# Performance work log

Hardware: AMD Instinct MI355X
Metric: run time of the kernel (lower is better)

## Reference

```python
import jax, jax.numpy as jnp
import numpy as np

B, T, N, F = 8, 64, 512, 32
G, C = 64, 64          # gcn_dim, tcn_dim
K, DIL = 2, 2          # TCN kernel_size, dilation
EPS = 1e-5


def setup_inputs() -> dict:
    key = jax.random.key(0)
    ks = jax.random.split(key, 20)
    s = 0.05
    return {
        "x": jax.random.normal(ks[0], (B, T, N, F), dtype=jnp.float32),
        "adj": jax.random.uniform(ks[1], (B, N, N), dtype=jnp.float32),
        # GraphConvLayer linear
        "gcn_w": jax.random.normal(ks[2], (F, G), dtype=jnp.float32) * s,
        "gcn_b": jnp.zeros((G,), dtype=jnp.float32),
        # TCN conv1 (weight-normed): v [out,in,K], g [out], bias [out]
        "v1": jax.random.normal(ks[3], (C, G, K), dtype=jnp.float32) * s,
        "g1": jnp.ones((C,), dtype=jnp.float32),
        "b1c": jnp.zeros((C,), dtype=jnp.float32),
        # TCN conv2
        "v2": jax.random.normal(ks[4], (C, C, K), dtype=jnp.float32) * s,
        "g2": jnp.ones((C,), dtype=jnp.float32),
        "b2c": jnp.zeros((C,), dtype=jnp.float32),
        # TemporalAttention: W1, W2 are [out,in] torch Linear layouts
        "W1": jax.random.normal(ks[5], (C, C), dtype=jnp.float32) * s,
        "b1": jnp.zeros((C,), dtype=jnp.float32),
        "W2": jax.random.normal(ks[6], (C, C), dtype=jnp.float32) * s,
        "b2": jnp.zeros((C,), dtype=jnp.float32),
        "Vw": jax.random.normal(ks[7], (C,), dtype=jnp.float32) * s,
        "Vb": jnp.zeros((), dtype=jnp.float32),
        # LayerNorm
        "ln_g": jnp.ones((C,), dtype=jnp.float32),
        "ln_b": jnp.zeros((C,), dtype=jnp.float32),
    }


def _wn(v, g):
    # torch weight_norm(dim=0): w = g * v / ||v|| over (in, K) per out-channel
    nrm = jnp.sqrt(jnp.sum(v * v, axis=(1, 2), keepdims=True))
    return g[:, None, None] * v / nrm


def _causal_conv(h, w, b, dilation):
    # h: [BN, Cin, T]; w: [Cout, Cin, K]; left-pad (K-1)*dilation == conv+chomp
    pad = (w.shape[2] - 1) * dilation
    y = jax.lax.conv_general_dilated(
        h, w, window_strides=(1,), padding=[(pad, 0)],
        rhs_dilation=(dilation,), dimension_numbers=("NCH", "OIH", "NCH"))
    return y + b[None, :, None]


def reference(x, adj, gcn_w, gcn_b, v1, g1, b1c, v2, g2, b2c,
              W1, b1, W2, b2, Vw, Vb, ln_g, ln_b):
    # ---- GCN (normalized adjacency is timestep-independent: compute once) ----
    adj_t = adj + jnp.eye(N, dtype=adj.dtype)[None]          # [B,N,N]
    deg = jnp.sum(adj_t, axis=2)                             # [B,N]
    d = jnp.where(deg > 0, jax.lax.rsqrt(jnp.where(deg > 0, deg, 1.0)), 0.0)
    norm_adj = d[:, :, None] * adj_t * d[:, None, :]         # [B,N,N]
    h = jnp.einsum("bij,btjf->btif", norm_adj, x)            # [B,T,N,F]
    gcn_out = jnp.einsum("btnf,fg->btng", h, gcn_w) + gcn_b  # [B,T,N,G]

    # ---- TCN over time, per (batch, node) channel sequence ----
    seq = gcn_out.transpose(0, 2, 3, 1).reshape(B * N, G, T)  # [BN,G,T]
    o1 = jax.nn.relu(_causal_conv(seq, _wn(v1, g1), b1c, DIL))
    o2 = jax.nn.relu(_causal_conv(o1, _wn(v2, g2), b2c, DIL))
    tcn = jax.nn.relu(o2 + seq)                               # shortcut=identity (G==C)
    tcn_out = tcn.reshape(B, N, C, T).transpose(0, 3, 1, 2)   # [B,T,N,C]

    # ---- Temporal attention per node (softmax over T) ----
    pre = jnp.tanh(jnp.einsum("btnc,dc->btnd", tcn_out, W1) + b1
                   + jnp.einsum("btnc,dc->btnd", tcn_out, W2) + b2)
    scores = jnp.einsum("btnd,d->btn", pre, Vw) + Vb          # [B,T,N]
    aw = jax.nn.softmax(scores, axis=1)                       # over T
    attn = jnp.einsum("btnc,btn->bnc", tcn_out, aw)           # [B,N,C]

    # ---- LayerNorm over channel dim ----
    mu = jnp.mean(attn, axis=-1, keepdims=True)
    var = jnp.mean((attn - mu) ** 2, axis=-1, keepdims=True)
    return (attn - mu) * jax.lax.rsqrt(var + EPS) * ln_g + ln_b
```

## Files before the change

kernel.cpp:

```cpp
#include <hip/hip_runtime.h>
#include <hip/hip_bf16.h>
#include <math.h>

#define B_ 8
#define T_ 64
#define N_ 512
#define F_ 32
#define G_ 64
#define C_ 64

typedef __attribute__((ext_vector_type(8))) short short8;
typedef __attribute__((ext_vector_type(4))) float f32x4;
typedef __attribute__((ext_vector_type(2))) float f32x2;

__device__ __forceinline__ unsigned short f2bf(float x) {
  unsigned u = __float_as_uint(x);
  u += 0x7fffu + ((u >> 16) & 1u);
  return (unsigned short)(u >> 16);
}
__device__ __forceinline__ float bf2f(unsigned short h) {
  return __uint_as_float(((unsigned)h) << 16);
}
__device__ __forceinline__ uint2 pack4(float a, float b, float c, float d) {
  uint2 r;
  r.x = (unsigned)f2bf(a) | ((unsigned)f2bf(b) << 16);
  r.y = (unsigned)f2bf(c) | ((unsigned)f2bf(d) << 16);
  return r;
}

__global__ __launch_bounds__(256) void deg_kernel(const float* __restrict__ adj,
                                                  float* __restrict__ d) {
  int row = blockIdx.x * 4 + (threadIdx.x >> 6);
  int lane = threadIdx.x & 63;
  const float* r = adj + (size_t)row * N_;
  float s = 0.f;
  #pragma unroll
  for (int j = lane; j < N_; j += 64) s += r[j];
  #pragma unroll
  for (int m = 1; m < 64; m <<= 1) s += __shfl_xor(s, m);
  if (lane == 0) {
    float deg = s + 1.0f;
    d[row] = (deg > 0.f) ? rsqrtf(deg) : 0.f;
  }
}

__global__ __launch_bounds__(256) void abf_kernel(const float* __restrict__ adj,
                                                  const float* __restrict__ d,
                                                  unsigned short* __restrict__ Abf) {
  int row = blockIdx.x * 4 + (threadIdx.x >> 6);
  int lane = threadIdx.x & 63;
  int b = row >> 9;
  int i = row & (N_ - 1);
  float di = d[row];
  const float* src = adj + (size_t)row * N_;
  unsigned short* dst = Abf + (size_t)row * N_;
  int j0 = lane * 8;
  float4 v0 = *(const float4*)(src + j0);
  float4 v1 = *(const float4*)(src + j0 + 4);
  float vals[8] = {v0.x, v0.y, v0.z, v0.w, v1.x, v1.y, v1.z, v1.w};
  unsigned short o[8];
  #pragma unroll
  for (int k = 0; k < 8; ++k) {
    int j = j0 + k;
    float a = vals[k] + ((i == j) ? 1.f : 0.f);
    o[k] = f2bf(a * di * d[b * N_ + j]);
  }
  uint4 pv;
  pv.x = (unsigned)o[0] | ((unsigned)o[1] << 16);
  pv.y = (unsigned)o[2] | ((unsigned)o[3] << 16);
  pv.z = (unsigned)o[4] | ((unsigned)o[5] << 16);
  pv.w = (unsigned)o[6] | ((unsigned)o[7] << 16);
  *(uint4*)(dst + j0) = pv;
}

__global__ __launch_bounds__(256) void xT_kernel(const float* __restrict__ x,
                                                 unsigned short* __restrict__ xT) {
  __shared__ float tile[64][33];
  int bt = blockIdx.x;
  int tid = threadIdx.x;
  const float* src = x + (size_t)bt * N_ * F_;
  unsigned short* dst = xT + (size_t)bt * F_ * N_;
  for (int j0 = 0; j0 < N_; j0 += 64) {
    #pragma unroll
    for (int kk = 0; kk < 2; ++kk) {
      int qq = tid + 256 * kk;
      int jl = qq >> 3, fc = qq & 7;
      float4 v = *(const float4*)(src + (size_t)(j0 + jl) * F_ + fc * 4);
      tile[jl][fc * 4 + 0] = v.x;
      tile[jl][fc * 4 + 1] = v.y;
      tile[jl][fc * 4 + 2] = v.z;
      tile[jl][fc * 4 + 3] = v.w;
    }
    __syncthreads();
    {
      int u = tid & 31, fr = tid >> 5;
      #pragma unroll
      for (int ff = 0; ff < 4; ++ff) {
        int f = fr + ff * 8;
        unsigned lo = f2bf(tile[2 * u][f]);
        unsigned hi = f2bf(tile[2 * u + 1][f]);
        ((unsigned*)(dst + (size_t)f * N_ + j0))[u] = lo | (hi << 16);
      }
    }
    __syncthreads();
  }
}

__global__ __launch_bounds__(256) void prep_kernel(
    const float* __restrict__ v1, const float* __restrict__ g1,
    const float* __restrict__ v2, const float* __restrict__ g2,
    const float* __restrict__ W1, const float* __restrict__ W2,
    const float* __restrict__ b1, const float* __restrict__ b2,
    const float* __restrict__ gcn_w,
    unsigned short* __restrict__ w1a, unsigned short* __restrict__ w1b,
    unsigned short* __restrict__ w2a, unsigned short* __restrict__ w2b,
    unsigned short* __restrict__ W12bf, float* __restrict__ b12,
    unsigned short* __restrict__ gw_bf) {
  int blk = blockIdx.x;
  int tid = threadIdx.x;
  if (blk < 128) {
    __shared__ float red[4];
    int c = blk & 63;
    const float* v = (blk < 64) ? v1 : v2;
    const float* g = (blk < 64) ? g1 : g2;
    unsigned short* wa = (blk < 64) ? w1a : w2a;
    unsigned short* wb = (blk < 64) ? w1b : w2b;
    float s = 0.f;
    if (tid < 128) { float t = v[c * 128 + tid]; s = t * t; }
    #pragma unroll
    for (int m = 1; m < 64; m <<= 1) s += __shfl_xor(s, m);
    if ((tid & 63) == 0) red[tid >> 6] = s;
    __syncthreads();
    float sc = g[c] / sqrtf(red[0] + red[1] + red[2] + red[3]);
    if (tid < 64) {
      int gg = tid;
      wa[c * 64 + gg] = f2bf(v[c * 128 + 2 * gg] * sc);
      wb[c * 64 + gg] = f2bf(v[c * 128 + 2 * gg + 1] * sc);
    }
  } else if (blk == 128) {
    for (int i = tid; i < 4096; i += 256) W12bf[i] = f2bf(W1[i] + W2[i]);
    if (tid < 64) b12[tid] = b1[tid] + b2[tid];
  } else {
    for (int i = tid; i < 2048; i += 256) {
      int g = i >> 5, f = i & 31;
      gw_bf[g * 32 + f] = f2bf(gcn_w[f * 64 + g]);
    }
  }
}

__global__ __launch_bounds__(256) void gcn_mfma_kernel(
    const unsigned short* __restrict__ Abf, const unsigned short* __restrict__ xT,
    unsigned short* __restrict__ h) {
  __shared__ unsigned short as_[64][40];
  __shared__ unsigned short xs_[64][40];

  int blk = blockIdx.x;
  int b = blk >> 8;
  int rem = blk & 255;
  int i0 = (rem >> 5) * 64;
  int t0 = (rem & 31) * 2;

  int tid = threadIdx.x;
  int l = tid & 63;
  int wq = tid >> 6;
  int wr = wq >> 1, wc = wq & 1;
  int lr = l & 15;
  int lk = (l >> 4) * 8;

  f32x4 acc00 = {0.f, 0.f, 0.f, 0.f}, acc01 = acc00, acc10 = acc00, acc11 = acc00;

  int srow = tid >> 2;
  int schunk = (tid & 3) * 8;

  const unsigned short* aSrc =
      Abf + ((size_t)(b * N_ + i0 + srow)) * N_ + schunk;
  int ttS = srow >> 5, fS = srow & 31;
  const unsigned short* xSrc =
      xT + ((size_t)((b * T_ + t0 + ttS) * F_ + fS)) * N_ + schunk;

  for (int j0 = 0; j0 < N_; j0 += 32) {
    *(short8*)&as_[srow][schunk] = *(const short8*)(aSrc + j0);
    *(short8*)&xs_[srow][schunk] = *(const short8*)(xSrc + j0);
    __syncthreads();
    short8 a0 = *(const short8*)&as_[wr * 32 + lr][lk];
    short8 a1 = *(const short8*)&as_[wr * 32 + 16 + lr][lk];
    short8 bb0 = *(const short8*)&xs_[wc * 32 + lr][lk];
    short8 bb1 = *(const short8*)&xs_[wc * 32 + 16 + lr][lk];
    acc00 = __builtin_amdgcn_mfma_f32_16x16x32_bf16(a0, bb0, acc00, 0, 0, 0);
    acc01 = __builtin_amdgcn_mfma_f32_16x16x32_bf16(a0, bb1, acc01, 0, 0, 0);
    acc10 = __builtin_amdgcn_mfma_f32_16x16x32_bf16(a1, bb0, acc10, 0, 0, 0);
    acc11 = __builtin_amdgcn_mfma_f32_16x16x32_bf16(a1, bb1, acc11, 0, 0, 0);
    __syncthreads();
  }

  int ibase = i0 + wr * 32 + (l >> 4) * 4;
  int cbase = wc * 32 + (l & 15);
  f32x4 accs[2][2] = {{acc00, acc01}, {acc10, acc11}};
  #pragma unroll
  for (int si = 0; si < 2; ++si)
    #pragma unroll
    for (int sc = 0; sc < 2; ++sc) {
      int col = cbase + sc * 16;
      int t = t0 + (col >> 5), f = col & 31;
      #pragma unroll
      for (int v = 0; v < 4; ++v) {
        int i = ibase + si * 16 + v;
        h[((size_t)((b * T_ + t) * N_ + i)) * F_ + f] = f2bf(accs[si][sc][v]);
      }
    }
}

__global__ __launch_bounds__(256) void tcn_attn_kernel(
    const unsigned short* __restrict__ h, const unsigned short* __restrict__ gw_bf,
    const float* __restrict__ gcn_b, const unsigned short* __restrict__ w1a,
    const unsigned short* __restrict__ w1b, const float* __restrict__ b1c,
    const unsigned short* __restrict__ w2a, const unsigned short* __restrict__ w2b,
    const float* __restrict__ b2c, const unsigned short* __restrict__ W12bf,
    const float* __restrict__ b12, const float* __restrict__ Vw,
    const float* __restrict__ Vb, const float* __restrict__ ln_g,
    const float* __restrict__ ln_b, float* __restrict__ out) {
  __shared__ unsigned short hS[64][40];
  __shared__ unsigned short seqS[66][72];
  __shared__ unsigned short o1S[66][72];
  __shared__ unsigned short tcnS[64][72];
  __shared__ float sp4[4][64];
  __shared__ float awS[64];

  int bn = blockIdx.x;
  int n = bn & (N_ - 1);
  int b = bn >> 9;
  int tid = threadIdx.x;
  int l = tid & 63;
  int q = tid >> 6;
  int lr = l & 15;
  int lk = (l >> 4) * 8;
  int c0 = q * 16 + (l >> 4) * 4;

  if (tid < 72) {
    seqS[0][tid] = 0; seqS[1][tid] = 0;
    o1S[0][tid] = 0;  o1S[1][tid] = 0;
  }
  {
    int t = tid >> 2, f0 = (tid & 3) * 8;
    *(short8*)&hS[t][f0] =
        *(const short8*)(h + ((size_t)((b * T_ + t) * N_ + n)) * F_ + f0);
  }
  __syncthreads();

  {
    short8 aG = *(const short8*)(gw_bf + (q * 16 + lr) * 32 + lk);
    float4 bias = *(const float4*)(gcn_b + c0);
    #pragma unroll
    for (int nt = 0; nt < 4; ++nt) {
      f32x4 acc = {0.f, 0.f, 0.f, 0.f};
      short8 bh = *(const short8*)&hS[nt * 16 + lr][lk];
      acc = __builtin_amdgcn_mfma_f32_16x16x32_bf16(aG, bh, acc, 0, 0, 0);
      uint2 pv = pack4(acc[0] + bias.x, acc[1] + bias.y,
                       acc[2] + bias.z, acc[3] + bias.w);
      *(uint2*)&seqS[nt * 16 + lr + 2][c0] = pv;
    }
  }
  __syncthreads();

  {
    short8 aA0 = *(const short8*)(w1a + (q * 16 + lr) * 64 + lk);
    short8 aA1 = *(const short8*)(w1a + (q * 16 + lr) * 64 + 32 + lk);
    short8 aB0 = *(const short8*)(w1b + (q * 16 + lr) * 64 + lk);
    short8 aB1 = *(const short8*)(w1b + (q * 16 + lr) * 64 + 32 + lk);
    float4 bias = *(const float4*)(b1c + c0);
    f32x4 acc[4];
    #pragma unroll
    for (int nt = 0; nt < 4; ++nt) acc[nt] = (f32x4){0.f, 0.f, 0.f, 0.f};
    #pragma unroll
    for (int nt = 0; nt < 4; ++nt) {
      int tr = nt * 16 + lr;
      short8 b00 = *(const short8*)&seqS[tr][lk];
      short8 b10 = *(const short8*)&seqS[tr + 2][lk];
      acc[nt] = __builtin_amdgcn_mfma_f32_16x16x32_bf16(aA0, b00, acc[nt], 0, 0, 0);
      acc[nt] = __builtin_amdgcn_mfma_f32_16x16x32_bf16(aB0, b10, acc[nt], 0, 0, 0);
    }
    #pragma unroll
    for (int nt = 0; nt < 4; ++nt) {
      int tr = nt * 16 + lr;
      short8 b01 = *(const short8*)&seqS[tr][32 + lk];
      short8 b11 = *(const short8*)&seqS[tr + 2][32 + lk];
      acc[nt] = __builtin_amdgcn_mfma_f32_16x16x32_bf16(aA1, b01, acc[nt], 0, 0, 0);
      acc[nt] = __builtin_amdgcn_mfma_f32_16x16x32_bf16(aB1, b11, acc[nt], 0, 0, 0);
    }
    #pragma unroll
    for (int nt = 0; nt < 4; ++nt) {
      uint2 pv = pack4(fmaxf(acc[nt][0] + bias.x, 0.f),
                       fmaxf(acc[nt][1] + bias.y, 0.f),
                       fmaxf(acc[nt][2] + bias.z, 0.f),
                       fmaxf(acc[nt][3] + bias.w, 0.f));
      *(uint2*)&o1S[nt * 16 + lr + 2][c0] = pv;
    }
  }
  __syncthreads();

  {
    short8 aA0 = *(const short8*)(w2a + (q * 16 + lr) * 64 + lk);
    short8 aA1 = *(const short8*)(w2a + (q * 16 + lr) * 64 + 32 + lk);
    short8 aB0 = *(const short8*)(w2b + (q * 16 + lr) * 64 + lk);
    short8 aB1 = *(const short8*)(w2b + (q * 16 + lr) * 64 + 32 + lk);
    float4 bias = *(const float4*)(b2c + c0);
    f32x4 acc[4];
    #pragma unroll
    for (int nt = 0; nt < 4; ++nt) acc[nt] = (f32x4){0.f, 0.f, 0.f, 0.f};
    #pragma unroll
    for (int nt = 0; nt < 4; ++nt) {
      int tr = nt * 16 + lr;
      short8 b00 = *(const short8*)&o1S[tr][lk];
      short8 b10 = *(const short8*)&o1S[tr + 2][lk];
      acc[nt] = __builtin_amdgcn_mfma_f32_16x16x32_bf16(aA0, b00, acc[nt], 0, 0, 0);
      acc[nt] = __builtin_amdgcn_mfma_f32_16x16x32_bf16(aB0, b10, acc[nt], 0, 0, 0);
    }
    #pragma unroll
    for (int nt = 0; nt < 4; ++nt) {
      int tr = nt * 16 + lr;
      short8 b01 = *(const short8*)&o1S[tr][32 + lk];
      short8 b11 = *(const short8*)&o1S[tr + 2][32 + lk];
      acc[nt] = __builtin_amdgcn_mfma_f32_16x16x32_bf16(aA1, b01, acc[nt], 0, 0, 0);
      acc[nt] = __builtin_amdgcn_mfma_f32_16x16x32_bf16(aB1, b11, acc[nt], 0, 0, 0);
    }
    #pragma unroll
    for (int nt = 0; nt < 4; ++nt) {
      int tr = nt * 16 + lr;
      uint2 sk = *(const uint2*)&seqS[tr + 2][c0];
      float s0 = bf2f((unsigned short)(sk.x & 0xffff));
      float s1 = bf2f((unsigned short)(sk.x >> 16));
      float s2 = bf2f((unsigned short)(sk.y & 0xffff));
      float s3 = bf2f((unsigned short)(sk.y >> 16));
      uint2 pv = pack4(fmaxf(fmaxf(acc[nt][0] + bias.x, 0.f) + s0, 0.f),
                       fmaxf(fmaxf(acc[nt][1] + bias.y, 0.f) + s1, 0.f),
                       fmaxf(fmaxf(acc[nt][2] + bias.z, 0.f) + s2, 0.f),
                       fmaxf(fmaxf(acc[nt][3] + bias.w, 0.f) + s3, 0.f));
      *(uint2*)&tcnS[tr][c0] = pv;
    }
  }
  __syncthreads();

  {
    short8 aW0 = *(const short8*)(W12bf + (q * 16 + lr) * 64 + lk);
    short8 aW1 = *(const short8*)(W12bf + (q * 16 + lr) * 64 + 32 + lk);
    float4 vwv = *(const float4*)(Vw + c0);
    float4 b12v = *(const float4*)(b12 + c0);
    #pragma unroll
    for (int nt = 0; nt < 4; ++nt) {
      int tr = nt * 16 + lr;
      f32x4 acc = {0.f, 0.f, 0.f, 0.f};
      short8 bb0 = *(const short8*)&tcnS[tr][lk];
      short8 bb1 = *(const short8*)&tcnS[tr][32 + lk];
      acc = __builtin_amdgcn_mfma_f32_16x16x32_bf16(aW0, bb0, acc, 0, 0, 0);
      acc = __builtin_amdgcn_mfma_f32_16x16x32_bf16(aW1, bb1, acc, 0, 0, 0);
      float p = 0.f;
      float bv[4] = {b12v.x, b12v.y, b12v.z, b12v.w};
      float vv[4] = {vwv.x, vwv.y, vwv.z, vwv.w};
      #pragma unroll
      for (int r = 0; r < 4; ++r) {
        float s = acc[r] + bv[r];
        float e = __expf(2.f * s);
        p += vv[r] * (1.f - 2.f / (e + 1.f));
      }
      p += __shfl_xor(p, 16);
      p += __shfl_xor(p, 32);
      if (l < 16) sp4[q][nt * 16 + l] = p;
    }
  }
  __syncthreads();

  if (tid < 64) {
    float s = sp4[0][l] + sp4[1][l] + sp4[2][l] + sp4[3][l] + Vb[0];
    float m = s;
    #pragma unroll
    for (int msk = 1; msk < 64; msk <<= 1) m = fmaxf(m, __shfl_xor(m, msk));
    float e = __expf(s - m);
    float su = e;
    #pragma unroll
    for (int msk = 1; msk < 64; msk <<= 1) su += __shfl_xor(su, msk);
    awS[l] = e / su;
  }
  __syncthreads();

  {
    float pa = 0.f;
    #pragma unroll
    for (int k = 0; k < 16; ++k)
      pa += bf2f(tcnS[q * 16 + k][l]) * awS[q * 16 + k];
    sp4[q][l] = pa;
  }
  __syncthreads();

  if (tid < 64) {
    int c = l;
    float a = sp4[0][c] + sp4[1][c] + sp4[2][c] + sp4[3][c];
    float su = a;
    #pragma unroll
    for (int msk = 1; msk < 64; msk <<= 1) su += __shfl_xor(su, msk);
    float mu = su * (1.f / 64.f);
    float dv = a - mu;
    float vv = dv * dv;
    #pragma unroll
    for (int msk = 1; msk < 64; msk <<= 1) vv += __shfl_xor(vv, msk);
    float rs = rsqrtf(vv * (1.f / 64.f) + 1e-5f);
    out[(size_t)bn * C_ + c] = dv * rs * ln_g[c] + ln_b[c];
  }
}

extern "C" void kernel_launch(void* const* d_in, const int* in_sizes, int n_in,
                              void* d_out, int out_size, void* d_ws, size_t ws_size,
                              hipStream_t stream) {
  (void)in_sizes; (void)n_in; (void)out_size; (void)ws_size;
  const float* x     = (const float*)d_in[0];
  const float* adj   = (const float*)d_in[1];
  const float* gcn_w = (const float*)d_in[2];
  const float* gcn_b = (const float*)d_in[3];
  const float* v1    = (const float*)d_in[4];
  const float* g1    = (const float*)d_in[5];
  const float* b1c   = (const float*)d_in[6];
  const float* v2    = (const float*)d_in[7];
  const float* g2    = (const float*)d_in[8];
  const float* b2c   = (const float*)d_in[9];
  const float* W1    = (const float*)d_in[10];
  const float* b1    = (const float*)d_in[11];
  const float* W2    = (const float*)d_in[12];
  const float* b2    = (const float*)d_in[13];
  const float* Vw    = (const float*)d_in[14];
  const float* Vb    = (const float*)d_in[15];
  const float* ln_g  = (const float*)d_in[16];
  const float* ln_b  = (const float*)d_in[17];
  float* out = (float*)d_out;

  char* ws = (char*)d_ws;
  unsigned short* h    = (unsigned short*)(ws);
  unsigned short* Abf  = (unsigned short*)(ws + 16777216);
  unsigned short* xT   = (unsigned short*)(ws + 20971520);
  float* dd            = (float*)(ws + 37748736);
  unsigned short* gw_bf= (unsigned short*)(ws + 37765120);
  unsigned short* w1a  = (unsigned short*)(ws + 37769216);
  unsigned short* w1b  = (unsigned short*)(ws + 37777408);
  unsigned short* w2a  = (unsigned short*)(ws + 37785600);
  unsigned short* w2b  = (unsigned short*)(ws + 37793792);
  unsigned short* W12bf= (unsigned short*)(ws + 37801984);
  float* b12           = (float*)(ws + 37810176);

  deg_kernel<<<(B_ * N_) / 4, 256, 0, stream>>>(adj, dd);
  abf_kernel<<<(B_ * N_) / 4, 256, 0, stream>>>(adj, dd, Abf);
  xT_kernel<<<B_ * T_, 256, 0, stream>>>(x, xT);
  prep_kernel<<<130, 256, 0, stream>>>(v1, g1, v2, g2, W1, W2, b1, b2, gcn_w,
                                       w1a, w1b, w2a, w2b, W12bf, b12, gw_bf);
  gcn_mfma_kernel<<<B_ * 256, 256, 0, stream>>>(Abf, xT, h);
  tcn_attn_kernel<<<B_ * N_, 256, 0, stream>>>(h, gw_bf, gcn_b, w1a, w1b, b1c,
                                               w2a, w2b, b2c, W12bf, b12, Vw,
                                               Vb, ln_g, ln_b, out);
}
```

Measured before the change: 187.3 us.

## Merge prep kernels, use direct global-to-LDS loads and packed bf16 converts

Folds the adjacency-normalisation, x-transpose and weight-prep kernels into one launch (1024+512+130 blocks), which removes two kernel launches and their serialization gaps. The GCN GEMM and TCN kernels now stage tiles with global_load_lds, skipping the register round trip, and LDS padding is dropped to fit that contiguous layout. Float-to-bf16 packing uses the hardware v_cvt_pk_bf16_f32 instruction. Unpadded LDS rows may add bank conflicts in the MFMA operand reads.

```diff
diff --git a/kernel.cpp b/kernel.cpp
--- a/kernel.cpp
+++ b/kernel.cpp
@@ -11,7 +11,6 @@
 
 typedef __attribute__((ext_vector_type(8))) short short8;
 typedef __attribute__((ext_vector_type(4))) float f32x4;
-typedef __attribute__((ext_vector_type(2))) float f32x2;
 
 __device__ __forceinline__ unsigned short f2bf(float x) {
   unsigned u = __float_as_uint(x);
@@ -21,12 +20,18 @@
 __device__ __forceinline__ float bf2f(unsigned short h) {
   return __uint_as_float(((unsigned)h) << 16);
 }
+__device__ __forceinline__ unsigned cvtpk(float lo, float hi) {
+  unsigned r;
+  asm("v_cvt_pk_bf16_f32 %0, %1, %2" : "=v"(r) : "v"(lo), "v"(hi));
+  return r;
+}
 __device__ __forceinline__ uint2 pack4(float a, float b, float c, float d) {
-  uint2 r;
-  r.x = (unsigned)f2bf(a) | ((unsigned)f2bf(b) << 16);
-  r.y = (unsigned)f2bf(c) | ((unsigned)f2bf(d) << 16);
-  return r;
-}
+  uint2 r; r.x = cvtpk(a, b); r.y = cvtpk(c, d); return r;
+}
+#define GLOAD16(gsrc, ldst)                                              \
+  __builtin_amdgcn_global_load_lds(                                      \
+      (const __attribute__((address_space(1))) unsigned int*)(gsrc),     \
+      (__attribute__((address_space(3))) unsigned int*)(ldst), 16, 0, 0)
 
 __global__ __launch_bounds__(256) void deg_kernel(const float* __restrict__ adj,
                                                   float* __restrict__ d) {
@@ -44,106 +49,104 @@
   }
 }
 
-__global__ __launch_bounds__(256) void abf_kernel(const float* __restrict__ adj,
-                                                  const float* __restrict__ d,
-                                                  unsigned short* __restrict__ Abf) {
-  int row = blockIdx.x * 4 + (threadIdx.x >> 6);
-  int lane = threadIdx.x & 63;
-  int b = row >> 9;
-  int i = row & (N_ - 1);
-  float di = d[row];
-  const float* src = adj + (size_t)row * N_;
-  unsigned short* dst = Abf + (size_t)row * N_;
-  int j0 = lane * 8;
-  float4 v0 = *(const float4*)(src + j0);
-  float4 v1 = *(const float4*)(src + j0 + 4);
-  float vals[8] = {v0.x, v0.y, v0.z, v0.w, v1.x, v1.y, v1.z, v1.w};
-  unsigned short o[8];
-  #pragma unroll
-  for (int k = 0; k < 8; ++k) {
-    int j = j0 + k;
-    float a = vals[k] + ((i == j) ? 1.f : 0.f);
-    o[k] = f2bf(a * di * d[b * N_ + j]);
-  }
-  uint4 pv;
-  pv.x = (unsigned)o[0] | ((unsigned)o[1] << 16);
-  pv.y = (unsigned)o[2] | ((unsigned)o[3] << 16);
-  pv.z = (unsigned)o[4] | ((unsigned)o[5] << 16);
-  pv.w = (unsigned)o[6] | ((unsigned)o[7] << 16);
-  *(uint4*)(dst + j0) = pv;
-}
-
-__global__ __launch_bounds__(256) void xT_kernel(const float* __restrict__ x,
-                                                 unsigned short* __restrict__ xT) {
-  __shared__ float tile[64][33];
-  int bt = blockIdx.x;
-  int tid = threadIdx.x;
-  const float* src = x + (size_t)bt * N_ * F_;
-  unsigned short* dst = xT + (size_t)bt * F_ * N_;
-  for (int j0 = 0; j0 < N_; j0 += 64) {
-    #pragma unroll
-    for (int kk = 0; kk < 2; ++kk) {
-      int qq = tid + 256 * kk;
-      int jl = qq >> 3, fc = qq & 7;
-      float4 v = *(const float4*)(src + (size_t)(j0 + jl) * F_ + fc * 4);
-      tile[jl][fc * 4 + 0] = v.x;
-      tile[jl][fc * 4 + 1] = v.y;
-      tile[jl][fc * 4 + 2] = v.z;
-      tile[jl][fc * 4 + 3] = v.w;
-    }
-    __syncthreads();
-    {
-      int u = tid & 31, fr = tid >> 5;
-      #pragma unroll
-      for (int ff = 0; ff < 4; ++ff) {
-        int f = fr + ff * 8;
-        unsigned lo = f2bf(tile[2 * u][f]);
-        unsigned hi = f2bf(tile[2 * u + 1][f]);
-        ((unsigned*)(dst + (size_t)f * N_ + j0))[u] = lo | (hi << 16);
-      }
-    }
-    __syncthreads();
-  }
-}
-
-__global__ __launch_bounds__(256) void prep_kernel(
+__global__ __launch_bounds__(256) void prep_all_kernel(
+    const float* __restrict__ adj, const float* __restrict__ d,
+    const float* __restrict__ x,
     const float* __restrict__ v1, const float* __restrict__ g1,
     const float* __restrict__ v2, const float* __restrict__ g2,
     const float* __restrict__ W1, const float* __restrict__ W2,
     const float* __restrict__ b1, const float* __restrict__ b2,
     const float* __restrict__ gcn_w,
+    unsigned short* __restrict__ Abf, unsigned short* __restrict__ xT,
     unsigned short* __restrict__ w1a, unsigned short* __restrict__ w1b,
     unsigned short* __restrict__ w2a, unsigned short* __restrict__ w2b,
     unsigned short* __restrict__ W12bf, float* __restrict__ b12,
     unsigned short* __restrict__ gw_bf) {
+  __shared__ float tile[64][33];
+  __shared__ float red[4];
   int blk = blockIdx.x;
   int tid = threadIdx.x;
-  if (blk < 128) {
-    __shared__ float red[4];
-    int c = blk & 63;
-    const float* v = (blk < 64) ? v1 : v2;
-    const float* g = (blk < 64) ? g1 : g2;
-    unsigned short* wa = (blk < 64) ? w1a : w2a;
-    unsigned short* wb = (blk < 64) ? w1b : w2b;
-    float s = 0.f;
-    if (tid < 128) { float t = v[c * 128 + tid]; s = t * t; }
-    #pragma unroll
-    for (int m = 1; m < 64; m <<= 1) s += __shfl_xor(s, m);
-    if ((tid & 63) == 0) red[tid >> 6] = s;
-    __syncthreads();
-    float sc = g[c] / sqrtf(red[0] + red[1] + red[2] + red[3]);
-    if (tid < 64) {
-      int gg = tid;
-      wa[c * 64 + gg] = f2bf(v[c * 128 + 2 * gg] * sc);
-      wb[c * 64 + gg] = f2bf(v[c * 128 + 2 * gg + 1] * sc);
-    }
-  } else if (blk == 128) {
-    for (int i = tid; i < 4096; i += 256) W12bf[i] = f2bf(W1[i] + W2[i]);
-    if (tid < 64) b12[tid] = b1[tid] + b2[tid];
+
+  if (blk < 1024) {
+    int row = blk * 4 + (tid >> 6);
+    int lane = tid & 63;
+    int b = row >> 9;
+    int i = row & (N_ - 1);
+    float di = d[row];
+    const float* src = adj + (size_t)row * N_;
+    unsigned short* dst = Abf + (size_t)row * N_;
+    int j0 = lane * 8;
+    float4 v0 = *(const float4*)(src + j0);
+    float4 v1v = *(const float4*)(src + j0 + 4);
+    float vals[8] = {v0.x, v0.y, v0.z, v0.w, v1v.x, v1v.y, v1v.z, v1v.w};
+    unsigned short o[8];
+    #pragma unroll
+    for (int k = 0; k < 8; ++k) {
+      int j = j0 + k;
+      float a = vals[k] + ((i == j) ? 1.f : 0.f);
+      o[k] = f2bf(a * di * d[b * N_ + j]);
+    }
+    uint4 pv;
+    pv.x = (unsigned)o[0] | ((unsigned)o[1] << 16);
+    pv.y = (unsigned)o[2] | ((unsigned)o[3] << 16);
+    pv.z = (unsigned)o[4] | ((unsigned)o[5] << 16);
+    pv.w = (unsigned)o[6] | ((unsigned)o[7] << 16);
+    *(uint4*)(dst + j0) = pv;
+  } else if (blk < 1536) {
+    int bt = blk - 1024;
+    const float* src = x + (size_t)bt * N_ * F_;
+    unsigned short* dst = xT + (size_t)bt * F_ * N_;
+    for (int j0 = 0; j0 < N_; j0 += 64) {
+      #pragma unroll
+      for (int kk = 0; kk < 2; ++kk) {
+        int qq = tid + 256 * kk;
+        int jl = qq >> 3, fc = qq & 7;
+        float4 v = *(const float4*)(src + (size_t)(j0 + jl) * F_ + fc * 4);
+        tile[jl][fc * 4 + 0] = v.x;
+        tile[jl][fc * 4 + 1] = v.y;
+        tile[jl][fc * 4 + 2] = v.z;
+        tile[jl][fc * 4 + 3] = v.w;
+      }
+      __syncthreads();
+      {
+        int u = tid & 31, fr = tid >> 5;
+        #pragma unroll
+        for (int ff = 0; ff < 4; ++ff) {
+          int f = fr + ff * 8;
+          ((unsigned*)(dst + (size_t)f * N_ + j0))[u] =
+              cvtpk(tile[2 * u][f], tile[2 * u + 1][f]);
+        }
+      }
+      __syncthreads();
+    }
   } else {
-    for (int i = tid; i < 2048; i += 256) {
-      int g = i >> 5, f = i & 31;
-      gw_bf[g * 32 + f] = f2bf(gcn_w[f * 64 + g]);
+    int pblk = blk - 1536;
+    if (pblk < 128) {
+      int c = pblk & 63;
+      const float* v = (pblk < 64) ? v1 : v2;
+      const float* g = (pblk < 64) ? g1 : g2;
+      unsigned short* wa = (pblk < 64) ? w1a : w2a;
+      unsigned short* wb = (pblk < 64) ? w1b : w2b;
+      float s = 0.f;
+      if (tid < 128) { float t = v[c * 128 + tid]; s = t * t; }
+      #pragma unroll
+      for (int m = 1; m < 64; m <<= 1) s += __shfl_xor(s, m);
+      if ((tid & 63) == 0) red[tid >> 6] = s;
+      __syncthreads();
+      float sc = g[c] / sqrtf(red[0] + red[1] + red[2] + red[3]);
+      if (tid < 64) {
+        int gg = tid;
+        wa[c * 64 + gg] = f2bf(v[c * 128 + 2 * gg] * sc);
+        wb[c * 64 + gg] = f2bf(v[c * 128 + 2 * gg + 1] * sc);
+      }
+    } else if (pblk == 128) {
+      for (int i = tid; i < 4096; i += 256) W12bf[i] = f2bf(W1[i] + W2[i]);
+      if (tid < 64) b12[tid] = b1[tid] + b2[tid];
+    } else {
+      for (int i = tid; i < 2048; i += 256) {
+        int g = i >> 5, f = i & 31;
+        gw_bf[g * 32 + f] = f2bf(gcn_w[f * 64 + g]);
+      }
     }
   }
 }
@@ -151,8 +154,8 @@
 __global__ __launch_bounds__(256) void gcn_mfma_kernel(
     const unsigned short* __restrict__ Abf, const unsigned short* __restrict__ xT,
     unsigned short* __restrict__ h) {
-  __shared__ unsigned short as_[64][40];
-  __shared__ unsigned short xs_[64][40];
+  __shared__ __align__(16) unsigned short as_[64][32];
+  __shared__ __align__(16) unsigned short xs_[64][32];
 
   int blk = blockIdx.x;
   int b = blk >> 8;
@@ -177,10 +180,12 @@
   int ttS = srow >> 5, fS = srow & 31;
   const unsigned short* xSrc =
       xT + ((size_t)((b * T_ + t0 + ttS) * F_ + fS)) * N_ + schunk;
+  unsigned short* aDst = &as_[0][0] + tid * 8;
+  unsigned short* xDst = &xs_[0][0] + tid * 8;
 
   for (int j0 = 0; j0 < N_; j0 += 32) {
-    *(short8*)&as_[srow][schunk] = *(const short8*)(aSrc + j0);
-    *(short8*)&xs_[srow][schunk] = *(const short8*)(xSrc + j0);
+    GLOAD16(aSrc + j0, aDst);
+    GLOAD16(xSrc + j0, xDst);
     __syncthreads();
     short8 a0 = *(const short8*)&as_[wr * 32 + lr][lk];
     short8 a1 = *(const short8*)&as_[wr * 32 + 16 + lr][lk];
@@ -219,10 +224,9 @@
     const float* __restrict__ b12, const float* __restrict__ Vw,
     const float* __restrict__ Vb, const float* __restrict__ ln_g,
     const float* __restrict__ ln_b, float* __restrict__ out) {
-  __shared__ unsigned short hS[64][40];
-  __shared__ unsigned short seqS[66][72];
-  __shared__ unsigned short o1S[66][72];
-  __shared__ unsigned short tcnS[64][72];
+  __shared__ __align__(16) unsigned short seqS[66][72];
+  __shared__ __align__(16) unsigned short o1S[66][72];
+  __shared__ __align__(16) unsigned short tcnS[64][72];
   __shared__ float sp4[4][64];
   __shared__ float awS[64];
 
@@ -236,14 +240,15 @@
   int lk = (l >> 4) * 8;
   int c0 = q * 16 + (l >> 4) * 4;
 
+  unsigned short* hS = &tcnS[0][0];
+
   if (tid < 72) {
     seqS[0][tid] = 0; seqS[1][tid] = 0;
     o1S[0][tid] = 0;  o1S[1][tid] = 0;
   }
   {
     int t = tid >> 2, f0 = (tid & 3) * 8;
-    *(short8*)&hS[t][f0] =
-        *(const short8*)(h + ((size_t)((b * T_ + t) * N_ + n)) * F_ + f0);
+    GLOAD16(h + ((size_t)((b * T_ + t) * N_ + n)) * F_ + f0, hS + tid * 8);
   }
   __syncthreads();
 
@@ -253,7 +258,7 @@
     #pragma unroll
     for (int nt = 0; nt < 4; ++nt) {
       f32x4 acc = {0.f, 0.f, 0.f, 0.f};
-      short8 bh = *(const short8*)&hS[nt * 16 + lr][lk];
+      short8 bh = *(const short8*)&hS[(nt * 16 + lr) * 32 + lk];
       acc = __builtin_amdgcn_mfma_f32_16x16x32_bf16(aG, bh, acc, 0, 0, 0);
       uint2 pv = pack4(acc[0] + bias.x, acc[1] + bias.y,
                        acc[2] + bias.z, acc[3] + bias.w);
@@ -445,10 +450,10 @@
   float* b12           = (float*)(ws + 37810176);
 
   deg_kernel<<<(B_ * N_) / 4, 256, 0, stream>>>(adj, dd);
-  abf_kernel<<<(B_ * N_) / 4, 256, 0, stream>>>(adj, dd, Abf);
-  xT_kernel<<<B_ * T_, 256, 0, stream>>>(x, xT);
-  prep_kernel<<<130, 256, 0, stream>>>(v1, g1, v2, g2, W1, W2, b1, b2, gcn_w,
-                                       w1a, w1b, w2a, w2b, W12bf, b12, gw_bf);
+  prep_all_kernel<<<1666, 256, 0, stream>>>(adj, dd, x, v1, g1, v2, g2,
+                                            W1, W2, b1, b2, gcn_w,
+                                            Abf, xT, w1a, w1b, w2a, w2b,
+                                            W12bf, b12, gw_bf);
   gcn_mfma_kernel<<<B_ * 256, 256, 0, stream>>>(Abf, xT, h);
   tcn_attn_kernel<<<B_ * N_, 256, 0, stream>>>(h, gw_bf, gcn_b, w1a, w1b, b1c,
                                                w2a, w2b, b2c, W12bf, b12, Vw,
```

New measurement: 170.1 us. 9.2% less time.
